# Optimization experiments

Measured on AMD Instinct MI355X. Metric: run time of the kernel, lower is better.

Reference implementation:

```python
import jax, jax.numpy as jnp
import numpy as np

LAMBDA = 0.1   # lambda_ init arg
RHO = 1.0      # ADMM penalty parameter
N_ITERS = 50   # fixed ADMM iteration count (replaces eps_rel/eps_abs stopping rule, jit-friendly)


def _admm_box_qp(Q1, P):
    """Solve, for every (b, n): min_x 0.5 x^T Q1[b] x + P[b,n]^T x  s.t. 0 <= x <= 1.
    Q1: [b, m, m] (shared across n, so factor once per b), P: [b, n, m]. Returns z: [b, n, m]."""
    b, n, m = P.shape
    M_inv = jnp.linalg.inv(Q1 + RHO * jnp.eye(m, dtype=Q1.dtype))  # [b, m, m]

    x0 = jnp.zeros((b, n, m), P.dtype)

    def step(carry, _):
        x, z, u = carry
        rhs = RHO * (z - u) - P                       # [b, n, m]
        x = jnp.einsum('bij,bnj->bni', M_inv, rhs)    # x-update: (Q1 + rho I) x = rhs
        z = jnp.clip(x + u, 0.0, 1.0)                 # z-update: projection onto box [lb, ub] = [0, 1]
        u = u + x - z                                 # dual update
        return (x, z, u), None

    (x, z, u), _ = jax.lax.scan(step, (x0, x0, x0), None, length=N_ITERS)
    return z


def reference(Q, V):
    b, n, d = Q.shape
    m = V.shape[1]
    V = V / m
    # Q1 = 2 V V^T : [b, m, m]
    Q1 = 2.0 * jnp.einsum('bmd,bkd->bmk', V, V)
    # P = -2 V Q^T + lambda/m : [b, n, m]  (avoid materializing the b*n stacked copies of Q1)
    P = -2.0 * jnp.einsum('bmd,bnd->bnm', V, Q) + LAMBDA / m
    x = _admm_box_qp(Q1, P)                           # [b, n, m] in [0, 1]
    xb = jnp.where(x > 0.5, 1.0, 0.0)                 # hard threshold
    coeffs = xb / (jnp.abs(xb).sum(axis=-1, keepdims=True) + 1e-10)
    return jnp.einsum('bnm,bmd->bnd', coeffs, V)


def setup_inputs() -> dict:
    key = jax.random.key(0)
    kq, kv = jax.random.split(key)
    Q = jax.random.normal(kq, (8, 2048, 128), dtype=jnp.float32)
    V = jax.random.normal(kv, (8, 128, 128), dtype=jnp.float32)
    return {"Q": Q, "V": V}
```

## Files before the change

kernel.cpp:

```cpp
#include <hip/hip_runtime.h>

#define NBATCH 8
#define NROWS 2048
#define MDIM 128
#define NITER 50
#define PSTR2 33
#define RSTR_R 136
#define WLSTR 104
#define XSTR 132

#define RH_B 0
#define RM_B 8704
#define RL_B 17408
#define WL_B 26112
#define CNT_B 52736
#define SMEM_BYTES 54784
#define PMAT_B 0
#define QST_B 32768
#define XB_B 0
#define CF_B 16896

typedef unsigned short ushort_t;
typedef __attribute__((ext_vector_type(8))) short bf16x8;
typedef __attribute__((ext_vector_type(8))) unsigned short us8;
typedef __attribute__((ext_vector_type(4))) unsigned short us4;
typedef __attribute__((ext_vector_type(4))) float f32x4;

__device__ __host__ __forceinline__ ushort_t f2bf(float f) {
  unsigned int u = __builtin_bit_cast(unsigned int, f);
  unsigned int r = (u + 0x7fffu + ((u >> 16) & 1u)) >> 16;
  return (ushort_t)r;
}
__device__ __forceinline__ float bf2f(ushort_t h) {
  unsigned int u = ((unsigned int)h) << 16;
  return __builtin_bit_cast(float, u);
}

__global__ __launch_bounds__(256) void mk_m64(const float* __restrict__ V,
                                              double* __restrict__ M,
                                              double* __restrict__ X0) {
  __shared__ double sA[16][130];
  __shared__ double sB[32][130];
  const int b = blockIdx.x >> 5, t = blockIdx.x & 31;
  const int i0 = (t >> 2) << 4, j0 = (t & 3) << 5;
  const float* Vb = V + b * MDIM * MDIM;
  const int tid = threadIdx.x;
  const double S = 1.0 / 128.0;
  for (int idx = tid; idx < 512; idx += 256) {
    const int r = idx >> 5, c4 = (idx & 31) << 2;
    float4 v = *(const float4*)(Vb + (i0 + r) * MDIM + c4);
    sA[r][c4 + 0] = v.x * S; sA[r][c4 + 1] = v.y * S;
    sA[r][c4 + 2] = v.z * S; sA[r][c4 + 3] = v.w * S;
  }
  for (int idx = tid; idx < 1024; idx += 256) {
    const int r = idx >> 5, c4 = (idx & 31) << 2;
    float4 w = *(const float4*)(Vb + (j0 + r) * MDIM + c4);
    sB[r][c4 + 0] = w.x * S; sB[r][c4 + 1] = w.y * S;
    sB[r][c4 + 2] = w.z * S; sB[r][c4 + 3] = w.w * S;
  }
  __syncthreads();
  const int tx = tid & 15, ty = tid >> 4;
  double acc0 = 0.0, acc1 = 0.0;
  for (int k = 0; k < 128; ++k) {
    const double a0 = sA[ty][k];
    const double b0 = sB[tx * 2 + 0][k], b1 = sB[tx * 2 + 1][k];
    acc0 = fma(a0, b0, acc0); acc1 = fma(a0, b1, acc1);
  }
  double* Mb = M + b * 16384;
  double* Xb = X0 + b * 16384;
#pragma unroll
  for (int j = 0; j < 2; ++j) {
    const int gi = i0 + ty, gj = j0 + tx * 2 + j;
    const double diag = (gi == gj) ? 1.0 : 0.0;
    const double mv = 2.0 * (j ? acc1 : acc0) + diag;
    Mb[gi * 128 + gj] = mv;
    Xb[gi * 128 + gj] = 2.0 * diag - mv;
  }
}

__global__ __launch_bounds__(256) void ns_gemm64(const double* __restrict__ A,
                                                 const double* __restrict__ B,
                                                 double* __restrict__ C,
                                                 const double* __restrict__ Xc,
                                                 int mode) {
  __shared__ double sA[16][130];
  __shared__ double sB[32][130];
  const int b = blockIdx.x >> 5, t = blockIdx.x & 31;
  const int i0 = (t >> 2) << 4, j0 = (t & 3) << 5;
  const double* Ab = A + b * 16384;
  const double* Bb = B + b * 16384;
  const int tid = threadIdx.x;
  for (int idx = tid; idx < 1024; idx += 256) {
    const int r = idx >> 6, c2 = (idx & 63) << 1;
    *(double2*)&sA[r][c2] = *(const double2*)(Ab + (i0 + r) * 128 + c2);
  }
  for (int idx = tid; idx < 2048; idx += 256) {
    const int r = idx >> 6, c2 = (idx & 63) << 1;
    *(double2*)&sB[r][c2] = *(const double2*)(Bb + (j0 + r) * 128 + c2);
  }
  __syncthreads();
  const int tx = tid & 15, ty = tid >> 4;
  double acc0 = 0.0, acc1 = 0.0;
  for (int k = 0; k < 128; ++k) {
    const double a0 = sA[ty][k];
    const double b0 = sB[tx * 2 + 0][k], b1 = sB[tx * 2 + 1][k];
    acc0 = fma(a0, b0, acc0); acc1 = fma(a0, b1, acc1);
  }
  double* Cb = C + b * 16384;
  const double* Xcb = Xc + b * 16384;
#pragma unroll
  for (int j = 0; j < 2; ++j) {
    const int gi = i0 + ty, gj = j0 + tx * 2 + j;
    double v = (j ? acc1 : acc0);
    if (mode != 0) v = 2.0 * Xcb[gi * 128 + gj] - v;
    Cb[gi * 128 + gj] = v;
  }
}

__global__ __launch_bounds__(256) void prep_aux(const double* __restrict__ Minv,
                                                const float* __restrict__ V,
                                                ushort_t* __restrict__ Whg,
                                                ushort_t* __restrict__ Wmg,
                                                ushort_t* __restrict__ Wlg,
                                                double* __restrict__ VsT64) {
  const int b = blockIdx.x >> 3, ch = blockIdx.x & 7;
  const double* Mb = Minv + b * 16384;
  const float* Vb = V + b * 16384;
  ushort_t* Whb = Whg + b * 16384;
  ushort_t* Wmb = Wmg + b * 16384;
  ushort_t* Wlb = Wlg + b * 16384;
  double* Tb = VsT64 + b * 16384;
  const int base = ch * 2048;
  for (int k = threadIdx.x; k < 2048; k += 256) {
    const int idx = base + k;
    const int j = idx >> 7, c = idx & 127;
    const double diag = (j == c) ? 1.0 : 0.0;
    const float wf = (float)(diag - Mb[idx]);
    const ushort_t h = f2bf(wf);
    const float r1 = wf - bf2f(h);
    const ushort_t m_ = f2bf(r1);
    const float r2 = r1 - bf2f(m_);
    const ushort_t l_ = f2bf(r2);
    Whb[c * 128 + j] = h;
    Wmb[c * 128 + j] = m_;
    Wlb[c * 128 + j] = l_;
    Tb[idx] = (double)Vb[c * 128 + j] * (1.0 / 128.0);
  }
}

__global__ __launch_bounds__(512, 4) void admm_mfma(const float* __restrict__ Q,
                                                    const float* __restrict__ V,
                                                    const ushort_t* __restrict__ Whg,
                                                    const ushort_t* __restrict__ Wmg,
                                                    const ushort_t* __restrict__ Wlg,
                                                    const double* __restrict__ VsT64,
                                                    float* __restrict__ out) {
  __shared__ __align__(16) char smem[SMEM_BYTES];
  const int tid = threadIdx.x;
  const int b = blockIdx.x & 7;
  const int n0 = (blockIdx.x >> 3) << 5;
  const int lane = tid & 63;
  const int w = tid >> 6;
  const int quad = lane >> 4, col16 = lane & 15;
  const int rowA = w * 16 + col16;
  const int nrow0 = col16;
  const int nrow1 = 16 + col16;
  const int cbase = w * 16 + quad * 4;
  const int row = lane & 31;
  const int chalf = lane >> 5;

  const float* Qb = Q + ((size_t)(b * NROWS + n0)) * MDIM;
  const float* Vw = V + b * 16384 + w * 16;
  const double* vtb = VsT64 + b * 16384 + w * 16;
  float* outb = out + ((size_t)(b * NROWS + n0)) * MDIM;
  const ushort_t* WG0 = Whg + b * 16384;
  const ushort_t* WG1 = Wmg + b * 16384;
  const ushort_t* WG2 = Wlg + b * 16384;

  float* QST = (float*)(smem + QST_B);
  double* pmat = (double*)(smem + PMAT_B);
  ushort_t* rhp = (ushort_t*)(smem + RH_B);
  ushort_t* rmp = (ushort_t*)(smem + RM_B);
  ushort_t* rlp = (ushort_t*)(smem + RL_B);
  ushort_t* wl = (ushort_t*)(smem + WL_B);
  float* sCnt = (float*)(smem + CNT_B);

  for (int idx = tid; idx < 1024; idx += 512) {
    const int r = idx >> 5, d4 = (idx & 31) << 2;
    const float4 q = *(const float4*)(Qb + r * 128 + d4);
    QST[(d4 + 0) * PSTR2 + r] = q.x;
    QST[(d4 + 1) * PSTR2 + r] = q.y;
    QST[(d4 + 2) * PSTR2 + r] = q.z;
    QST[(d4 + 3) * PSTR2 + r] = q.w;
  }
  __syncthreads();

  double p8[8];
#pragma unroll
  for (int c = 0; c < 8; ++c) p8[c] = 0.0;
  for (int d = 0; d < 128; ++d) {
    const double a = (double)QST[d * PSTR2 + row];
    const double* vt = vtb + d * 128;
#pragma unroll
    for (int c = 0; c < 8; ++c) {
      const double vv = chalf ? vt[8 + c] : vt[c];
      p8[c] = fma(a, vv, p8[c]);
    }
  }
  const double LAM = 0.1 / 128.0;
#pragma unroll
  for (int c = 0; c < 8; ++c) p8[c] = fma(-2.0, p8[c], LAM);
#pragma unroll
  for (int c = 0; c < 8; ++c) pmat[row * 128 + w * 16 + chalf * 8 + c] = p8[c];
  __syncthreads();

  double pC[2][4];
#pragma unroll
  for (int i = 0; i < 4; ++i) {
    pC[0][i] = pmat[nrow0 * 128 + cbase + i];
    pC[1][i] = pmat[nrow1 * 128 + cbase + i];
  }
  __syncthreads();

  for (int idx = tid; idx < 1536; idx += 512) {
    const int c = idx / 12, t8 = idx - c * 12;
    *(us8*)(wl + c * WLSTR + t8 * 8) = *(const us8*)(WG2 + c * 128 + 32 + t8 * 8);
  }
  bf16x8 wfh[4], wfm[4];
#pragma unroll
  for (int ks = 0; ks < 4; ++ks) {
    wfh[ks] = *(const bf16x8*)(WG0 + rowA * 128 + ks * 32 + quad * 8);
    wfm[ks] = *(const bf16x8*)(WG1 + rowA * 128 + ks * 32 + quad * 8);
  }
  const bf16x8 wf0l = *(const bf16x8*)(WG2 + rowA * 128 + quad * 8);
  __syncthreads();

  double z[2][4], u[2][4];
#pragma unroll
  for (int t = 0; t < 2; ++t)
#pragma unroll
    for (int i = 0; i < 4; ++i) { z[t][i] = 0.0; u[t][i] = 0.0; }

  for (int it = 0; it < NITER; ++it) {
#pragma unroll
    for (int t = 0; t < 2; ++t) {
      const int nr = t ? nrow1 : nrow0;
      us4 hh, mm2, ll;
#pragma unroll
      for (int i = 0; i < 4; ++i) {
        const double rv = (z[t][i] - u[t][i]) - pC[t][i];
        const float rf = (float)rv;
        const ushort_t h = f2bf(rf);
        const float r1 = rf - bf2f(h);
        const ushort_t m_ = f2bf(r1);
        const float r2 = r1 - bf2f(m_);
        const ushort_t l_ = f2bf(r2);
        hh[i] = h; mm2[i] = m_; ll[i] = l_;
      }
      *(us4*)(rhp + nr * RSTR_R + cbase) = hh;
      *(us4*)(rmp + nr * RSTR_R + cbase) = mm2;
      *(us4*)(rlp + nr * RSTR_R + cbase) = ll;
    }
    __syncthreads();

    f32x4 acc0 = {0.f, 0.f, 0.f, 0.f};
    f32x4 acc1 = {0.f, 0.f, 0.f, 0.f};
#pragma unroll
    for (int ks = 0; ks < 4; ++ks) {
      const bf16x8 ah = wfh[ks];
      const bf16x8 am2 = wfm[ks];
      const bf16x8 al2 = (ks == 0)
          ? wf0l
          : *(const bf16x8*)(wl + rowA * WLSTR + (ks - 1) * 32 + quad * 8);
      const int kq = ks * 32 + quad * 8;
      {
        const bf16x8 bh = *(const bf16x8*)(rhp + nrow0 * RSTR_R + kq);
        const bf16x8 bm = *(const bf16x8*)(rmp + nrow0 * RSTR_R + kq);
        const bf16x8 bl = *(const bf16x8*)(rlp + nrow0 * RSTR_R + kq);
        acc0 = __builtin_amdgcn_mfma_f32_16x16x32_bf16(ah,  bh, acc0, 0, 0, 0);
        acc0 = __builtin_amdgcn_mfma_f32_16x16x32_bf16(ah,  bm, acc0, 0, 0, 0);
        acc0 = __builtin_amdgcn_mfma_f32_16x16x32_bf16(am2, bh, acc0, 0, 0, 0);
        acc0 = __builtin_amdgcn_mfma_f32_16x16x32_bf16(am2, bm, acc0, 0, 0, 0);
        acc0 = __builtin_amdgcn_mfma_f32_16x16x32_bf16(ah,  bl, acc0, 0, 0, 0);
        acc0 = __builtin_amdgcn_mfma_f32_16x16x32_bf16(al2, bh, acc0, 0, 0, 0);
      }
      {
        const bf16x8 bh = *(const bf16x8*)(rhp + nrow1 * RSTR_R + kq);
        const bf16x8 bm = *(const bf16x8*)(rmp + nrow1 * RSTR_R + kq);
        const bf16x8 bl = *(const bf16x8*)(rlp + nrow1 * RSTR_R + kq);
        acc1 = __builtin_amdgcn_mfma_f32_16x16x32_bf16(ah,  bh, acc1, 0, 0, 0);
        acc1 = __builtin_amdgcn_mfma_f32_16x16x32_bf16(ah,  bm, acc1, 0, 0, 0);
        acc1 = __builtin_amdgcn_mfma_f32_16x16x32_bf16(am2, bh, acc1, 0, 0, 0);
        acc1 = __builtin_amdgcn_mfma_f32_16x16x32_bf16(am2, bm, acc1, 0, 0, 0);
        acc1 = __builtin_amdgcn_mfma_f32_16x16x32_bf16(ah,  bl, acc1, 0, 0, 0);
        acc1 = __builtin_amdgcn_mfma_f32_16x16x32_bf16(al2, bh, acc1, 0, 0, 0);
      }
    }
    __syncthreads();

#pragma unroll
    for (int t = 0; t < 2; ++t)
#pragma unroll
      for (int i = 0; i < 4; ++i) {
        const float corr = (t == 0) ? acc0[i] : acc1[i];
        const double rv = (z[t][i] - u[t][i]) - pC[t][i];
        const double x = rv - (double)corr;
        const double y = x + u[t][i];
        const double zn = fmin(fmax(y, 0.0), 1.0);
        u[t][i] = y - zn;
        z[t][i] = zn;
      }
  }

  float* xbm = (float*)(smem + XB_B);
#pragma unroll
  for (int t = 0; t < 2; ++t) {
    const int nr = t ? nrow1 : nrow0;
    float4 o;
    o.x = (z[t][0] > 0.5) ? 1.f : 0.f;
    o.y = (z[t][1] > 0.5) ? 1.f : 0.f;
    o.z = (z[t][2] > 0.5) ? 1.f : 0.f;
    o.w = (z[t][3] > 0.5) ? 1.f : 0.f;
    *(float4*)(xbm + nr * XSTR + cbase) = o;
  }
  __syncthreads();

  const int c8 = w * 16 + chalf * 8;
  float xb8[8];
  {
    const float4 a = *(const float4*)(xbm + row * XSTR + c8 + 0);
    const float4 c2 = *(const float4*)(xbm + row * XSTR + c8 + 4);
    xb8[0] = a.x; xb8[1] = a.y; xb8[2] = a.z; xb8[3] = a.w;
    xb8[4] = c2.x; xb8[5] = c2.y; xb8[6] = c2.z; xb8[7] = c2.w;
  }
  double cnt = 0.0;
#pragma unroll
  for (int c = 0; c < 8; ++c) cnt += (double)xb8[c];
  sCnt[(w * 2 + chalf) * 32 + row] = (float)cnt;
  __syncthreads();
  double k = 0.0;
#pragma unroll
  for (int g = 0; g < 16; ++g) k += (double)sCnt[g * 32 + row];
  const double rkS = (1.0 / 128.0) / (k + 1e-10);
  float* cf = (float*)(smem + CF_B);
  {
    float4 w0, w1;
    w0.x = (float)((double)xb8[0] * rkS); w0.y = (float)((double)xb8[1] * rkS);
    w0.z = (float)((double)xb8[2] * rkS); w0.w = (float)((double)xb8[3] * rkS);
    w1.x = (float)((double)xb8[4] * rkS); w1.y = (float)((double)xb8[5] * rkS);
    w1.z = (float)((double)xb8[6] * rkS); w1.w = (float)((double)xb8[7] * rkS);
    *(float4*)(cf + row * XSTR + c8 + 0) = w0;
    *(float4*)(cf + row * XSTR + c8 + 4) = w1;
  }
  __syncthreads();

  float oa[8];
#pragma unroll
  for (int c = 0; c < 8; ++c) oa[c] = 0.f;
#pragma unroll 4
  for (int m4 = 0; m4 < 32; ++m4) {
    const float4 a4 = *(const float4*)(cf + row * XSTR + (m4 << 2));
#pragma unroll
    for (int mm = 0; mm < 4; ++mm) {
      const int m = (m4 << 2) + mm;
      const float* vp = Vw + m * 128;
      const float am = (mm == 0) ? a4.x : (mm == 1) ? a4.y : (mm == 2) ? a4.z : a4.w;
#pragma unroll
      for (int c = 0; c < 8; ++c) {
        const float vv = chalf ? vp[8 + c] : vp[c];
        oa[c] = fmaf(am, vv, oa[c]);
      }
    }
  }
#pragma unroll
  for (int q = 0; q < 2; ++q) {
    float4 o;
    o.x = oa[q * 4 + 0]; o.y = oa[q * 4 + 1];
    o.z = oa[q * 4 + 2]; o.w = oa[q * 4 + 3];
    *(float4*)(outb + row * 128 + c8 + q * 4) = o;
  }
}

extern "C" void kernel_launch(void* const* d_in, const int* in_sizes, int n_in,
                              void* d_out, int out_size, void* d_ws, size_t ws_size,
                              hipStream_t stream) {
  const float* Q = (const float*)d_in[0];
  const float* V = (const float*)d_in[1];
  float* out = (float*)d_out;
  double* ws = (double*)d_ws;
  double* Mw = ws;
  double* Xa = ws + 131072;
  double* Xb = ws + 262144;
  double* Tw = ws + 393216;

  mk_m64<<<256, 256, 0, stream>>>(V, Mw, Xa);
  double* pa = Xa;
  double* pb = Xb;
  for (int i = 0; i < 3; ++i) {
    ns_gemm64<<<256, 256, 0, stream>>>(pa, Mw, Tw, pa, 0);
    ns_gemm64<<<256, 256, 0, stream>>>(Tw, pa, pb, pa, 1);
    double* tmp = pa; pa = pb; pb = tmp;
  }
  ushort_t* Whg = (ushort_t*)Mw;
  ushort_t* Wmg = Whg + 131072;
  ushort_t* Wlg = Whg + 262144;
  double* VsT64 = Tw;
  prep_aux<<<64, 256, 0, stream>>>(pa, V, Whg, Wmg, Wlg, VsT64);
  admm_mfma<<<512, 512, 0, stream>>>(Q, V, Whg, Wmg, Wlg, VsT64, out);
}
```

Baseline: 323.6 us.

## Retile ADMM kernel to 64-row blocks with 32x32 MFMA and split-K reduction

The ADMM kernel now handles 64 rows per 1024-thread block. Each wave computes a 32x32 output tile with 32x32x16 bf16 MFMAs over half of K, and the two halves are combined through an LDS reduction buffer. The bf16 three-way split of the inverse is fused into the last Newton-Schulz GEMM, and the V-transpose prep moves into mk_m64 when the workspace is large enough, which removes the separate prep kernel launch. In exchange the LDS footprint grows to about 132KB per block, which limits the kernel to one block per CU, and each iteration gains an extra reduction step with a barrier.

Measured after the change: 478.1 us. 47.7% more time.

```diff
diff --git a/kernel.cpp b/kernel.cpp
--- a/kernel.cpp
+++ b/kernel.cpp
@@ -1,32 +1,31 @@
 #include <hip/hip_runtime.h>
 
-#define NBATCH 8
 #define NROWS 2048
 #define MDIM 128
 #define NITER 50
-#define PSTR2 33
-#define RSTR_R 136
-#define WLSTR 104
+#define PSTR 65
+#define RSTR 136
 #define XSTR 132
 
 #define RH_B 0
-#define RM_B 8704
-#define RL_B 17408
-#define WL_B 26112
-#define CNT_B 52736
-#define SMEM_BYTES 54784
-#define PMAT_B 0
-#define QST_B 32768
+#define RM_B 17408
+#define RL_B 34816
+#define WL_B 52224
+#define RED_B 87040
+#define CNT_B 128000
+#define SMEM_BYTES 132096
+#define QST_B 0
+#define PMAT_B 33792
 #define XB_B 0
-#define CF_B 16896
+#define CF_B 33792
 
 typedef unsigned short ushort_t;
 typedef __attribute__((ext_vector_type(8))) short bf16x8;
 typedef __attribute__((ext_vector_type(8))) unsigned short us8;
 typedef __attribute__((ext_vector_type(4))) unsigned short us4;
-typedef __attribute__((ext_vector_type(4))) float f32x4;
-
-__device__ __host__ __forceinline__ ushort_t f2bf(float f) {
+typedef __attribute__((ext_vector_type(16))) float f32x16;
+
+__device__ __forceinline__ ushort_t f2bf(float f) {
   unsigned int u = __builtin_bit_cast(unsigned int, f);
   unsigned int r = (u + 0x7fffu + ((u >> 16) & 1u)) >> 16;
   return (ushort_t)r;
@@ -38,7 +37,8 @@
 
 __global__ __launch_bounds__(256) void mk_m64(const float* __restrict__ V,
                                               double* __restrict__ M,
-                                              double* __restrict__ X0) {
+                                              double* __restrict__ X0,
+                                              double* __restrict__ vs) {
   __shared__ double sA[16][130];
   __shared__ double sB[32][130];
   const int b = blockIdx.x >> 5, t = blockIdx.x & 31;
@@ -58,6 +58,15 @@
     sB[r][c4 + 0] = w.x * S; sB[r][c4 + 1] = w.y * S;
     sB[r][c4 + 2] = w.z * S; sB[r][c4 + 3] = w.w * S;
   }
+  if (vs) {
+    double* Tb = vs + b * 16384;
+    const int base2 = t * 512;
+    for (int k = tid; k < 512; k += 256) {
+      const int idx = base2 + k;
+      const int j = idx >> 7, c = idx & 127;
+      Tb[idx] = (double)Vb[c * 128 + j] * (1.0 / 128.0);
+    }
+  }
   __syncthreads();
   const int tx = tid & 15, ty = tid >> 4;
   double acc0 = 0.0, acc1 = 0.0;
@@ -82,7 +91,10 @@
                                                  const double* __restrict__ B,
                                                  double* __restrict__ C,
                                                  const double* __restrict__ Xc,
-                                                 int mode) {
+                                                 int mode,
+                                                 ushort_t* __restrict__ Whg,
+                                                 ushort_t* __restrict__ Wmg,
+                                                 ushort_t* __restrict__ Wlg) {
   __shared__ double sA[16][130];
   __shared__ double sB[32][130];
   const int b = blockIdx.x >> 5, t = blockIdx.x & 31;
@@ -114,234 +126,216 @@
     double v = (j ? acc1 : acc0);
     if (mode != 0) v = 2.0 * Xcb[gi * 128 + gj] - v;
     Cb[gi * 128 + gj] = v;
-  }
-}
-
-__global__ __launch_bounds__(256) void prep_aux(const double* __restrict__ Minv,
-                                                const float* __restrict__ V,
-                                                ushort_t* __restrict__ Whg,
-                                                ushort_t* __restrict__ Wmg,
-                                                ushort_t* __restrict__ Wlg,
-                                                double* __restrict__ VsT64) {
+    if (mode == 2) {
+      const double diag = (gi == gj) ? 1.0 : 0.0;
+      const float wf = (float)(diag - v);
+      const ushort_t h = f2bf(wf);
+      const float r1 = wf - bf2f(h);
+      const ushort_t m_ = f2bf(r1);
+      const float r2 = r1 - bf2f(m_);
+      const ushort_t l_ = f2bf(r2);
+      Whg[b * 16384 + gj * 128 + gi] = h;
+      Wmg[b * 16384 + gj * 128 + gi] = m_;
+      Wlg[b * 16384 + gj * 128 + gi] = l_;
+    }
+  }
+}
+
+__global__ __launch_bounds__(256) void vst_prep(const float* __restrict__ V,
+                                                double* __restrict__ vs) {
   const int b = blockIdx.x >> 3, ch = blockIdx.x & 7;
-  const double* Mb = Minv + b * 16384;
   const float* Vb = V + b * 16384;
-  ushort_t* Whb = Whg + b * 16384;
-  ushort_t* Wmb = Wmg + b * 16384;
-  ushort_t* Wlb = Wlg + b * 16384;
-  double* Tb = VsT64 + b * 16384;
+  double* Tb = vs + b * 16384;
   const int base = ch * 2048;
   for (int k = threadIdx.x; k < 2048; k += 256) {
     const int idx = base + k;
     const int j = idx >> 7, c = idx & 127;
-    const double diag = (j == c) ? 1.0 : 0.0;
-    const float wf = (float)(diag - Mb[idx]);
-    const ushort_t h = f2bf(wf);
-    const float r1 = wf - bf2f(h);
-    const ushort_t m_ = f2bf(r1);
-    const float r2 = r1 - bf2f(m_);
-    const ushort_t l_ = f2bf(r2);
-    Whb[c * 128 + j] = h;
-    Wmb[c * 128 + j] = m_;
-    Wlb[c * 128 + j] = l_;
     Tb[idx] = (double)Vb[c * 128 + j] * (1.0 / 128.0);
   }
 }
 
-__global__ __launch_bounds__(512, 4) void admm_mfma(const float* __restrict__ Q,
-                                                    const float* __restrict__ V,
-                                                    const ushort_t* __restrict__ Whg,
-                                                    const ushort_t* __restrict__ Wmg,
-                                                    const ushort_t* __restrict__ Wlg,
-                                                    const double* __restrict__ VsT64,
-                                                    float* __restrict__ out) {
+__global__ __launch_bounds__(1024, 4) void admm_mfma(const float* __restrict__ Q,
+                                                     const float* __restrict__ V,
+                                                     const ushort_t* __restrict__ Whg,
+                                                     const ushort_t* __restrict__ Wmg,
+                                                     const ushort_t* __restrict__ Wlg,
+                                                     const double* __restrict__ VsT64,
+                                                     float* __restrict__ out) {
   __shared__ __align__(16) char smem[SMEM_BYTES];
   const int tid = threadIdx.x;
   const int b = blockIdx.x & 7;
-  const int n0 = (blockIdx.x >> 3) << 5;
+  const int n0 = (blockIdx.x >> 3) << 6;
   const int lane = tid & 63;
   const int w = tid >> 6;
-  const int quad = lane >> 4, col16 = lane & 15;
-  const int rowA = w * 16 + col16;
-  const int nrow0 = col16;
-  const int nrow1 = 16 + col16;
-  const int cbase = w * 16 + quad * 4;
-  const int row = lane & 31;
-  const int chalf = lane >> 5;
+  const int half = w >> 3;
+  const int p = w & 7;
+  const int ct = p & 3, nt = p >> 2;
+  const int l5 = lane & 31, kh = lane >> 5;
+  const int nloc = 32 * nt + l5;
+  const int cB = 32 * ct + 16 * half + 4 * kh;
+  const int k0 = 64 * half;
 
   const float* Qb = Q + ((size_t)(b * NROWS + n0)) * MDIM;
-  const float* Vw = V + b * 16384 + w * 16;
-  const double* vtb = VsT64 + b * 16384 + w * 16;
   float* outb = out + ((size_t)(b * NROWS + n0)) * MDIM;
-  const ushort_t* WG0 = Whg + b * 16384;
-  const ushort_t* WG1 = Wmg + b * 16384;
-  const ushort_t* WG2 = Wlg + b * 16384;
+  const ushort_t* WhB = Whg + b * 16384;
+  const ushort_t* WmB = Wmg + b * 16384;
+  const ushort_t* WlB = Wlg + b * 16384;
 
   float* QST = (float*)(smem + QST_B);
   double* pmat = (double*)(smem + PMAT_B);
   ushort_t* rhp = (ushort_t*)(smem + RH_B);
   ushort_t* rmp = (ushort_t*)(smem + RM_B);
   ushort_t* rlp = (ushort_t*)(smem + RL_B);
-  ushort_t* wl = (ushort_t*)(smem + WL_B);
+  ushort_t* wlp = (ushort_t*)(smem + WL_B);
+  float* red = (float*)(smem + RED_B);
   float* sCnt = (float*)(smem + CNT_B);
 
-  for (int idx = tid; idx < 1024; idx += 512) {
+  for (int idx = tid; idx < 2048; idx += 1024) {
     const int r = idx >> 5, d4 = (idx & 31) << 2;
     const float4 q = *(const float4*)(Qb + r * 128 + d4);
-    QST[(d4 + 0) * PSTR2 + r] = q.x;
-    QST[(d4 + 1) * PSTR2 + r] = q.y;
-    QST[(d4 + 2) * PSTR2 + r] = q.z;
-    QST[(d4 + 3) * PSTR2 + r] = q.w;
-  }
-  __syncthreads();
-
-  double p8[8];
-#pragma unroll
-  for (int c = 0; c < 8; ++c) p8[c] = 0.0;
-  for (int d = 0; d < 128; ++d) {
-    const double a = (double)QST[d * PSTR2 + row];
-    const double* vt = vtb + d * 128;
-#pragma unroll
-    for (int c = 0; c < 8; ++c) {
-      const double vv = chalf ? vt[8 + c] : vt[c];
-      p8[c] = fma(a, vv, p8[c]);
-    }
-  }
-  const double LAM = 0.1 / 128.0;
-#pragma unroll
-  for (int c = 0; c < 8; ++c) p8[c] = fma(-2.0, p8[c], LAM);
-#pragma unroll
-  for (int c = 0; c < 8; ++c) pmat[row * 128 + w * 16 + chalf * 8 + c] = p8[c];
-  __syncthreads();
-
-  double pC[2][4];
-#pragma unroll
-  for (int i = 0; i < 4; ++i) {
-    pC[0][i] = pmat[nrow0 * 128 + cbase + i];
-    pC[1][i] = pmat[nrow1 * 128 + cbase + i];
-  }
-  __syncthreads();
-
-  for (int idx = tid; idx < 1536; idx += 512) {
-    const int c = idx / 12, t8 = idx - c * 12;
-    *(us8*)(wl + c * WLSTR + t8 * 8) = *(const us8*)(WG2 + c * 128 + 32 + t8 * 8);
+    QST[(d4 + 0) * PSTR + r] = q.x;
+    QST[(d4 + 1) * PSTR + r] = q.y;
+    QST[(d4 + 2) * PSTR + r] = q.z;
+    QST[(d4 + 3) * PSTR + r] = q.w;
+  }
+  __syncthreads();
+
+  {
+    const int r2 = tid & 63;
+    const int c8 = (tid >> 6) << 3;
+    const double* vtb = VsT64 + b * 16384 + c8;
+    double p8[8];
+#pragma unroll
+    for (int c = 0; c < 8; ++c) p8[c] = 0.0;
+    for (int d = 0; d < 128; ++d) {
+      const double a = (double)QST[d * PSTR + r2];
+      const double* vt = vtb + d * 128;
+#pragma unroll
+      for (int c = 0; c < 8; ++c) p8[c] = fma(a, vt[c], p8[c]);
+    }
+    const double LAM = 0.1 / 128.0;
+#pragma unroll
+    for (int c = 0; c < 8; ++c) p8[c] = fma(-2.0, p8[c], LAM);
+#pragma unroll
+    for (int c = 0; c < 8; ++c) pmat[r2 * 128 + c8 + c] = p8[c];
+  }
+  __syncthreads();
+
+  double pC[8];
+#pragma unroll
+  for (int s = 0; s < 8; ++s)
+    pC[s] = pmat[nloc * 128 + cB + (s & 3) + 8 * (s >> 2)];
+  __syncthreads();
+
+  for (int idx = tid; idx < 2048; idx += 1024) {
+    const int c = idx >> 4, g = idx & 15;
+    *(us8*)(wlp + c * RSTR + g * 8) = *(const us8*)(WlB + c * 128 + g * 8);
   }
   bf16x8 wfh[4], wfm[4];
 #pragma unroll
-  for (int ks = 0; ks < 4; ++ks) {
-    wfh[ks] = *(const bf16x8*)(WG0 + rowA * 128 + ks * 32 + quad * 8);
-    wfm[ks] = *(const bf16x8*)(WG1 + rowA * 128 + ks * 32 + quad * 8);
-  }
-  const bf16x8 wf0l = *(const bf16x8*)(WG2 + rowA * 128 + quad * 8);
-  __syncthreads();
-
-  double z[2][4], u[2][4];
-#pragma unroll
-  for (int t = 0; t < 2; ++t)
-#pragma unroll
-    for (int i = 0; i < 4; ++i) { z[t][i] = 0.0; u[t][i] = 0.0; }
+  for (int s = 0; s < 4; ++s) {
+    const int ko = (32 * ct + l5) * 128 + k0 + 16 * s + 8 * kh;
+    wfh[s] = *(const bf16x8*)(WhB + ko);
+    wfm[s] = *(const bf16x8*)(WmB + ko);
+  }
+  __syncthreads();
+
+  double z[8], u[8];
+#pragma unroll
+  for (int s = 0; s < 8; ++s) { z[s] = 0.0; u[s] = 0.0; }
+  const int rrow = nloc * RSTR;
+  const int wlrow = (32 * ct + l5) * RSTR;
+  float* slot = red + (p * 64 + lane) * 20;
 
   for (int it = 0; it < NITER; ++it) {
-#pragma unroll
-    for (int t = 0; t < 2; ++t) {
-      const int nr = t ? nrow1 : nrow0;
-      us4 hh, mm2, ll;
+    us4 h0, h1, m0, m1, l0, l1;
+#pragma unroll
+    for (int s = 0; s < 8; ++s) {
+      const double rv = (z[s] - u[s]) - pC[s];
+      const float rf = (float)rv;
+      const ushort_t hh = f2bf(rf);
+      const float r1 = rf - bf2f(hh);
+      const ushort_t mm = f2bf(r1);
+      const float r2 = r1 - bf2f(mm);
+      const ushort_t ll = f2bf(r2);
+      if (s < 4) { h0[s] = hh; m0[s] = mm; l0[s] = ll; }
+      else       { h1[s - 4] = hh; m1[s - 4] = mm; l1[s - 4] = ll; }
+    }
+    *(us4*)(rhp + rrow + cB) = h0;  *(us4*)(rhp + rrow + cB + 8) = h1;
+    *(us4*)(rmp + rrow + cB) = m0;  *(us4*)(rmp + rrow + cB + 8) = m1;
+    *(us4*)(rlp + rrow + cB) = l0;  *(us4*)(rlp + rrow + cB + 8) = l1;
+    __syncthreads();
+
+    f32x16 acc;
+#pragma unroll
+    for (int i = 0; i < 16; ++i) acc[i] = 0.f;
+#pragma unroll
+    for (int s = 0; s < 4; ++s) {
+      const int kq = k0 + 16 * s + 8 * kh;
+      const bf16x8 bh = *(const bf16x8*)(rhp + rrow + kq);
+      const bf16x8 bm = *(const bf16x8*)(rmp + rrow + kq);
+      const bf16x8 bl = *(const bf16x8*)(rlp + rrow + kq);
+      const bf16x8 al = *(const bf16x8*)(wlp + wlrow + kq);
+      acc = __builtin_amdgcn_mfma_f32_32x32x16_bf16(wfh[s], bh, acc, 0, 0, 0);
+      acc = __builtin_amdgcn_mfma_f32_32x32x16_bf16(wfh[s], bm, acc, 0, 0, 0);
+      acc = __builtin_amdgcn_mfma_f32_32x32x16_bf16(wfm[s], bh, acc, 0, 0, 0);
+      acc = __builtin_amdgcn_mfma_f32_32x32x16_bf16(wfm[s], bm, acc, 0, 0, 0);
+      acc = __builtin_amdgcn_mfma_f32_32x32x16_bf16(wfh[s], bl, acc, 0, 0, 0);
+      acc = __builtin_amdgcn_mfma_f32_32x32x16_bf16(al,     bh, acc, 0, 0, 0);
+    }
+    {
+      const int o = 8 * (1 - half);
+      float* dst = slot + (1 - half) * 8;
 #pragma unroll
       for (int i = 0; i < 4; ++i) {
-        const double rv = (z[t][i] - u[t][i]) - pC[t][i];
-        const float rf = (float)rv;
-        const ushort_t h = f2bf(rf);
-        const float r1 = rf - bf2f(h);
-        const ushort_t m_ = f2bf(r1);
-        const float r2 = r1 - bf2f(m_);
-        const ushort_t l_ = f2bf(r2);
-        hh[i] = h; mm2[i] = m_; ll[i] = l_;
+        float2 v2; v2.x = acc[o + 2 * i]; v2.y = acc[o + 2 * i + 1];
+        *(float2*)(dst + 2 * i) = v2;
       }
-      *(us4*)(rhp + nr * RSTR_R + cbase) = hh;
-      *(us4*)(rmp + nr * RSTR_R + cbase) = mm2;
-      *(us4*)(rlp + nr * RSTR_R + cbase) = ll;
     }
     __syncthreads();
-
-    f32x4 acc0 = {0.f, 0.f, 0.f, 0.f};
-    f32x4 acc1 = {0.f, 0.f, 0.f, 0.f};
-#pragma unroll
-    for (int ks = 0; ks < 4; ++ks) {
-      const bf16x8 ah = wfh[ks];
-      const bf16x8 am2 = wfm[ks];
-      const bf16x8 al2 = (ks == 0)
-          ? wf0l
-          : *(const bf16x8*)(wl + rowA * WLSTR + (ks - 1) * 32 + quad * 8);
-      const int kq = ks * 32 + quad * 8;
-      {
-        const bf16x8 bh = *(const bf16x8*)(rhp + nrow0 * RSTR_R + kq);
-        const bf16x8 bm = *(const bf16x8*)(rmp + nrow0 * RSTR_R + kq);
-        const bf16x8 bl = *(const bf16x8*)(rlp + nrow0 * RSTR_R + kq);
-        acc0 = __builtin_amdgcn_mfma_f32_16x16x32_bf16(ah,  bh, acc0, 0, 0, 0);
-        acc0 = __builtin_amdgcn_mfma_f32_16x16x32_bf16(ah,  bm, acc0, 0, 0, 0);
-        acc0 = __builtin_amdgcn_mfma_f32_16x16x32_bf16(am2, bh, acc0, 0, 0, 0);
-        acc0 = __builtin_amdgcn_mfma_f32_16x16x32_bf16(am2, bm, acc0, 0, 0, 0);
-        acc0 = __builtin_amdgcn_mfma_f32_16x16x32_bf16(ah,  bl, acc0, 0, 0, 0);
-        acc0 = __builtin_amdgcn_mfma_f32_16x16x32_bf16(al2, bh, acc0, 0, 0, 0);
-      }
-      {
-        const bf16x8 bh = *(const bf16x8*)(rhp + nrow1 * RSTR_R + kq);
-        const bf16x8 bm = *(const bf16x8*)(rmp + nrow1 * RSTR_R + kq);
-        const bf16x8 bl = *(const bf16x8*)(rlp + nrow1 * RSTR_R + kq);
-        acc1 = __builtin_amdgcn_mfma_f32_16x16x32_bf16(ah,  bh, acc1, 0, 0, 0);
-        acc1 = __builtin_amdgcn_mfma_f32_16x16x32_bf16(ah,  bm, acc1, 0, 0, 0);
-        acc1 = __builtin_amdgcn_mfma_f32_16x16x32_bf16(am2, bh, acc1, 0, 0, 0);
-        acc1 = __builtin_amdgcn_mfma_f32_16x16x32_bf16(am2, bm, acc1, 0, 0, 0);
-        acc1 = __builtin_amdgcn_mfma_f32_16x16x32_bf16(ah,  bl, acc1, 0, 0, 0);
-        acc1 = __builtin_amdgcn_mfma_f32_16x16x32_bf16(al2, bh, acc1, 0, 0, 0);
-      }
-    }
-    __syncthreads();
-
-#pragma unroll
-    for (int t = 0; t < 2; ++t)
-#pragma unroll
-      for (int i = 0; i < 4; ++i) {
-        const float corr = (t == 0) ? acc0[i] : acc1[i];
-        const double rv = (z[t][i] - u[t][i]) - pC[t][i];
-        const double x = rv - (double)corr;
-        const double y = x + u[t][i];
-        const double zn = fmin(fmax(y, 0.0), 1.0);
-        u[t][i] = y - zn;
-        z[t][i] = zn;
-      }
+    const float* rs = slot + half * 8;
+    const int o2 = 8 * half;
+#pragma unroll
+    for (int s = 0; s < 8; ++s) {
+      const float corr = acc[o2 + s] + rs[s];
+      const double rv = (z[s] - u[s]) - pC[s];
+      const double x = rv - (double)corr;
+      const double y = x + u[s];
+      const double zn = fmin(fmax(y, 0.0), 1.0);
+      u[s] = y - zn;
+      z[s] = zn;
+    }
   }
 
   float* xbm = (float*)(smem + XB_B);
-#pragma unroll
-  for (int t = 0; t < 2; ++t) {
-    const int nr = t ? nrow1 : nrow0;
-    float4 o;
-    o.x = (z[t][0] > 0.5) ? 1.f : 0.f;
-    o.y = (z[t][1] > 0.5) ? 1.f : 0.f;
-    o.z = (z[t][2] > 0.5) ? 1.f : 0.f;
-    o.w = (z[t][3] > 0.5) ? 1.f : 0.f;
-    *(float4*)(xbm + nr * XSTR + cbase) = o;
-  }
-  __syncthreads();
-
-  const int c8 = w * 16 + chalf * 8;
+  {
+    float4 x0, x1;
+    x0.x = (z[0] > 0.5) ? 1.f : 0.f; x0.y = (z[1] > 0.5) ? 1.f : 0.f;
+    x0.z = (z[2] > 0.5) ? 1.f : 0.f; x0.w = (z[3] > 0.5) ? 1.f : 0.f;
+    x1.x = (z[4] > 0.5) ? 1.f : 0.f; x1.y = (z[5] > 0.5) ? 1.f : 0.f;
+    x1.z = (z[6] > 0.5) ? 1.f : 0.f; x1.w = (z[7] > 0.5) ? 1.f : 0.f;
+    *(float4*)(xbm + nloc * XSTR + cB) = x0;
+    *(float4*)(xbm + nloc * XSTR + cB + 8) = x1;
+  }
+  __syncthreads();
+
+  const int n2 = tid >> 4, cg = tid & 15;
   float xb8[8];
   {
-    const float4 a = *(const float4*)(xbm + row * XSTR + c8 + 0);
-    const float4 c2 = *(const float4*)(xbm + row * XSTR + c8 + 4);
+    const float4 a = *(const float4*)(xbm + n2 * XSTR + 8 * cg + 0);
+    const float4 c2 = *(const float4*)(xbm + n2 * XSTR + 8 * cg + 4);
     xb8[0] = a.x; xb8[1] = a.y; xb8[2] = a.z; xb8[3] = a.w;
     xb8[4] = c2.x; xb8[5] = c2.y; xb8[6] = c2.z; xb8[7] = c2.w;
   }
   double cnt = 0.0;
 #pragma unroll
   for (int c = 0; c < 8; ++c) cnt += (double)xb8[c];
-  sCnt[(w * 2 + chalf) * 32 + row] = (float)cnt;
-  __syncthreads();
-  double k = 0.0;
-#pragma unroll
-  for (int g = 0; g < 16; ++g) k += (double)sCnt[g * 32 + row];
-  const double rkS = (1.0 / 128.0) / (k + 1e-10);
+  sCnt[n2 * 16 + cg] = (float)cnt;
+  __syncthreads();
+  double kk = 0.0;
+#pragma unroll
+  for (int g = 0; g < 16; ++g) kk += (double)sCnt[n2 * 16 + g];
+  const double rkS = (1.0 / 128.0) / (kk + 1e-10);
   float* cf = (float*)(smem + CF_B);
   {
     float4 w0, w1;
@@ -349,27 +343,26 @@
     w0.z = (float)((double)xb8[2] * rkS); w0.w = (float)((double)xb8[3] * rkS);
     w1.x = (float)((double)xb8[4] * rkS); w1.y = (float)((double)xb8[5] * rkS);
     w1.z = (float)((double)xb8[6] * rkS); w1.w = (float)((double)xb8[7] * rkS);
-    *(float4*)(cf + row * XSTR + c8 + 0) = w0;
-    *(float4*)(cf + row * XSTR + c8 + 4) = w1;
-  }
-  __syncthreads();
-
+    *(float4*)(cf + n2 * XSTR + 8 * cg + 0) = w0;
+    *(float4*)(cf + n2 * XSTR + 8 * cg + 4) = w1;
+  }
+  __syncthreads();
+
+  const int n3 = tid & 63;
+  const int c8o = (tid >> 6) << 3;
+  const float* Vw = V + b * 16384 + c8o;
   float oa[8];
 #pragma unroll
   for (int c = 0; c < 8; ++c) oa[c] = 0.f;
 #pragma unroll 4
   for (int m4 = 0; m4 < 32; ++m4) {
-    const float4 a4 = *(const float4*)(cf + row * XSTR + (m4 << 2));
+    const float4 a4 = *(const float4*)(cf + n3 * XSTR + (m4 << 2));
 #pragma unroll
     for (int mm = 0; mm < 4; ++mm) {
-      const int m = (m4 << 2) + mm;
-      const float* vp = Vw + m * 128;
+      const float* vp = Vw + ((m4 << 2) + mm) * 128;
       const float am = (mm == 0) ? a4.x : (mm == 1) ? a4.y : (mm == 2) ? a4.z : a4.w;
 #pragma unroll
-      for (int c = 0; c < 8; ++c) {
-        const float vv = chalf ? vp[8 + c] : vp[c];
-        oa[c] = fmaf(am, vv, oa[c]);
-      }
+      for (int c = 0; c < 8; ++c) oa[c] = fmaf(am, vp[c], oa[c]);
     }
   }
 #pragma unroll
@@ -377,7 +370,7 @@
     float4 o;
     o.x = oa[q * 4 + 0]; o.y = oa[q * 4 + 1];
     o.z = oa[q * 4 + 2]; o.w = oa[q * 4 + 3];
-    *(float4*)(outb + row * 128 + c8 + q * 4) = o;
+    *(float4*)(outb + n3 * 128 + c8o + q * 4) = o;
   }
 }
 
@@ -392,19 +385,22 @@
   double* Xa = ws + 131072;
   double* Xb = ws + 262144;
   double* Tw = ws + 393216;
-
-  mk_m64<<<256, 256, 0, stream>>>(V, Mw, Xa);
+  ushort_t* Whg = (ushort_t*)Mw;
+  ushort_t* Wmg = Whg + 131072;
+  ushort_t* Wlg = Whg + 262144;
+
+  const bool big = ws_size >= (size_t)(5 * 1024 * 1024);
+  double* VsT = big ? (ws + 524288) : Tw;
+
+  mk_m64<<<256, 256, 0, stream>>>(V, Mw, Xa, big ? VsT : (double*)nullptr);
   double* pa = Xa;
   double* pb = Xb;
   for (int i = 0; i < 3; ++i) {
-    ns_gemm64<<<256, 256, 0, stream>>>(pa, Mw, Tw, pa, 0);
-    ns_gemm64<<<256, 256, 0, stream>>>(Tw, pa, pb, pa, 1);
+    ns_gemm64<<<256, 256, 0, stream>>>(pa, Mw, Tw, pa, 0, nullptr, nullptr, nullptr);
+    ns_gemm64<<<256, 256, 0, stream>>>(Tw, pa, pb, pa, (i == 2) ? 2 : 1,
+                                       Whg, Wmg, Wlg);
     double* tmp = pa; pa = pb; pb = tmp;
   }
-  ushort_t* Whg = (ushort_t*)Mw;
-  ushort_t* Wmg = Whg + 131072;
-  ushort_t* Wlg = Whg + 262144;
-  double* VsT64 = Tw;
-  prep_aux<<<64, 256, 0, stream>>>(pa, V, Whg, Wmg, Wlg, VsT64);
-  admm_mfma<<<512, 512, 0, stream>>>(Q, V, Whg, Wmg, Wlg, VsT64, out);
-}
+  if (!big) vst_prep<<<64, 256, 0, stream>>>(V, Tw);
+  admm_mfma<<<256, 1024, 0, stream>>>(Q, V, Whg, Wmg, Wlg, VsT, out);
+}
```
